# Optimization experiments

Measured on AMD Instinct MI355X. Metric: run time of the kernel, lower is better.

Reference implementation:

```python
import jax, jax.numpy as jnp
import numpy as np

EPS = 1e-16


def _euclidean_distance(x):
    # 'Euclidean Distance Matrix Trick' with the exact eps/mask handling of the torch code
    x2 = jnp.matmul(x, x.T)                      # [N, N]
    x2_norm = jnp.diag(x2)                       # [N]
    d = x2_norm[None, :] + x2_norm[:, None] - 2.0 * x2
    d = jax.nn.relu(d)
    mask = (d == 0.0).astype(d.dtype)
    d = d + mask * EPS
    d = jnp.sqrt(d + EPS) * (1.0 - mask) + EPS
    return d


def _valid_triplet_mask(labels):
    n = labels.shape[0]
    not_eye = ~jnp.eye(n, dtype=bool)            # [N, N]
    # distinct indices: i!=j, i!=k, j!=k
    distinct = not_eye[:, :, None] & not_eye[:, None, :] & not_eye[None, :, :]
    same = labels[None, :] == labels[:, None]    # [N, N]
    # label(i)==label(j) and label(i)!=label(k)
    valid = same[:, :, None] & ~same[:, None, :]
    return distinct & valid


def setup_inputs() -> dict:
    key = jax.random.key(0)
    k1, k2 = jax.random.split(key)
    N, D = 512, 128
    embeddings = jax.random.normal(k1, (N, D), dtype=jnp.float32)
    labels = jax.random.randint(k2, (N,), 0, 64, dtype=jnp.int64)
    bias = jnp.zeros((1,), dtype=jnp.float32)
    return {"embeddings": embeddings, "labels": labels, "bias": bias}


def reference(embeddings, labels, bias):
    distance = _euclidean_distance(embeddings)           # [N, N]
    # loss[i,j,k] = d(i,j) - d(i,k) + bias
    loss = distance[:, :, None] - distance[:, None, :] + bias[0]
    mask = _valid_triplet_mask(labels).astype(loss.dtype)
    loss = jax.nn.relu(loss * mask)
    num_positives = jnp.sum(loss > 1e-16).astype(loss.dtype)
    return jnp.sum(loss) / (num_positives + 1e-16)
```

## Files before the change

kernel.cpp:

```cpp
#include <hip/hip_runtime.h>

#define NPTS 512
#define DIM  128
#define EPSF 1e-16f
#define SROW 132

__global__ __launch_bounds__(512) void distmat(
    const float* __restrict__ X,
    float* __restrict__ D)
{
    __shared__ float A[32 * SROW];
    __shared__ float B[32 * SROW];
    __shared__ float nA[32], nB[32];

    const int bi = blockIdx.x & 15;
    const int bj = blockIdx.x >> 4;
    const int r0 = bi * 32, c0 = bj * 32;
    const int t = threadIdx.x;

    for (int g = t; g < 1024; g += 512) {
        const int r = g >> 5, c4 = g & 31;
        *reinterpret_cast<float4*>(&A[r * SROW + c4 * 4]) =
            reinterpret_cast<const float4*>(X + (size_t)(r0 + r) * DIM)[c4];
        *reinterpret_cast<float4*>(&B[r * SROW + c4 * 4]) =
            reinterpret_cast<const float4*>(X + (size_t)(c0 + r) * DIM)[c4];
    }
    __syncthreads();

    if (t < 64) {
        const float* src = (t < 32) ? &A[t * SROW] : &B[(t - 32) * SROW];
        float s = 0.f;
        for (int c4 = 0; c4 < 32; ++c4) {
            float4 v = *reinterpret_cast<const float4*>(src + c4 * 4);
            s += v.x * v.x + v.y * v.y + v.z * v.z + v.w * v.w;
        }
        if (t < 32) nA[t] = s; else nB[t - 32] = s;
    }
    __syncthreads();

    const int c  = t & 31;
    const int ty = t >> 5;
    float acc[2] = {0.f, 0.f};
    for (int k4 = 0; k4 < 32; ++k4) {
        const float4 bv = *reinterpret_cast<const float4*>(&B[c * SROW + k4 * 4]);
#pragma unroll
        for (int q = 0; q < 2; ++q) {
            const float4 av = *reinterpret_cast<const float4*>(&A[(ty + 16 * q) * SROW + k4 * 4]);
            acc[q] += av.x * bv.x + av.y * bv.y + av.z * bv.z + av.w * bv.w;
        }
    }
#pragma unroll
    for (int q = 0; q < 2; ++q) {
        const int r = ty + 16 * q;
        const float draw = fmaxf(nA[r] + nB[c] - 2.f * acc[q], 0.f);
        D[(size_t)(r0 + r) * NPTS + (c0 + c)] =
            (draw == 0.f) ? EPSF : (sqrtf(draw + EPSF) + EPSF);
    }
}

__global__ __launch_bounds__(512) void triplet_sum(
    const float* __restrict__ D,
    const int* __restrict__ labels,
    const float* __restrict__ bias,
    float* __restrict__ psum,
    unsigned* __restrict__ pcnt)
{
    __shared__ int      lab[NPTS];
    __shared__ float    drow[2][NPTS];
    __shared__ int      poslist[2][96];
    __shared__ int      npos[2];
    __shared__ float    wsum[8];
    __shared__ unsigned wcnt[8];

    const int blk = blockIdx.x;
    const int t   = threadIdx.x;
    const int i0  = blk * 2;

    lab[t] = labels[t];
    if (t < 256) {
        reinterpret_cast<float4*>(&drow[0][0])[t] =
            reinterpret_cast<const float4*>(D + (size_t)i0 * NPTS)[t];
    }
    if (t < 2) npos[t] = 0;
    __syncthreads();

    const int li0 = lab[i0], li1 = lab[i0 + 1];
    {
        const int j = t;
        if (lab[j] == li0 && j != i0)     { int q = atomicAdd(&npos[0], 1); poslist[0][q] = j; }
        if (lab[j] == li1 && j != i0 + 1) { int q = atomicAdd(&npos[1], 1); poslist[1][q] = j; }
    }
    __syncthreads();
    if (t < 2) {
        const int n = npos[t];
        for (int a2 = 1; a2 < n; ++a2) {
            int v = poslist[t][a2];
            int b2 = a2 - 1;
            while (b2 >= 0 && poslist[t][b2] > v) { poslist[t][b2 + 1] = poslist[t][b2]; --b2; }
            poslist[t][b2 + 1] = v;
        }
    }
    __syncthreads();

    const float bv = bias[0];
    float    lsum = 0.f;
    unsigned lcnt = 0u;
#pragma unroll
    for (int a = 0; a < 2; ++a) {
        const int   la = lab[i0 + a];
        const float* dr = &drow[a][0];
        if (lab[t] != la) {
            const float dik = dr[t];
            const int n = npos[a];
            for (int q = 0; q < n; ++q) {
                const float s = dr[poslist[a][q]] - dik + bv;
                if (s > 0.f) { lsum += s; lcnt += (s > EPSF) ? 1u : 0u; }
            }
        }
    }

#pragma unroll
    for (int off = 32; off > 0; off >>= 1) {
        lsum += __shfl_down(lsum, off);
        lcnt += __shfl_down(lcnt, off);
    }
    if ((t & 63) == 0) { wsum[t >> 6] = lsum; wcnt[t >> 6] = lcnt; }
    __syncthreads();
    if (t == 0) {
        float s = 0.f; unsigned c = 0u;
#pragma unroll
        for (int w = 0; w < 8; ++w) { s += wsum[w]; c += wcnt[w]; }
        psum[blk] = s;
        pcnt[blk] = c;
    }
}

__global__ __launch_bounds__(256) void triplet_finalize(
    const float* __restrict__ psum,
    const unsigned* __restrict__ pcnt,
    float* __restrict__ out)
{
    __shared__ float    ss[256];
    __shared__ unsigned sc[256];
    const int t = threadIdx.x;
    ss[t] = psum[t];
    sc[t] = pcnt[t];
    __syncthreads();
    for (int off = 128; off > 0; off >>= 1) {
        if (t < off) { ss[t] += ss[t + off]; sc[t] += sc[t + off]; }
        __syncthreads();
    }
    if (t == 0) out[0] = ss[0] / ((float)sc[0] + 1e-16f);
}

extern "C" void kernel_launch(void* const* d_in, const int* in_sizes, int n_in,
                              void* d_out, int out_size, void* d_ws, size_t ws_size,
                              hipStream_t stream) {
    const float* X      = (const float*)d_in[0];
    const int*   labels = (const int*)d_in[1];
    const float* bias   = (const float*)d_in[2];
    float*       out    = (float*)d_out;

    float*    D    = (float*)d_ws;
    float*    psum = (float*)((char*)d_ws + NPTS * NPTS * 4);
    unsigned* pcnt = (unsigned*)((char*)psum + 256 * 4);

    distmat<<<256, 512, 0, stream>>>(X, D);
    triplet_sum<<<256, 512, 0, stream>>>(D, labels, bias, psum, pcnt);
    triplet_finalize<<<1, 256, 0, stream>>>(psum, pcnt, out);
}
```

Before: 21.75 us.

## Fuse distance-matrix computation into triplet kernel and shuffle-reduce finalize

Removes the separate distmat kernel and global distance matrix; each triplet block now computes its two distance rows directly from X, using 4 threads per column j with shuffle reductions. This drops one launch and the write and re-read of a 1 MB matrix. In exchange each block re-reads all of X (256 KB, L2-resident) and recomputes the column norms, so total FLOPs are duplicated across blocks. The finalize kernel is also reduced to a single wavefront using shuffles instead of a shared-memory tree.

```diff
diff --git a/kernel.cpp b/kernel.cpp
--- a/kernel.cpp
+++ b/kernel.cpp
@@ -3,63 +3,9 @@
 #define NPTS 512
 #define DIM  128
 #define EPSF 1e-16f
-#define SROW 132
 
-__global__ __launch_bounds__(512) void distmat(
+__global__ __launch_bounds__(512) void triplet_fused(
     const float* __restrict__ X,
-    float* __restrict__ D)
-{
-    __shared__ float A[32 * SROW];
-    __shared__ float B[32 * SROW];
-    __shared__ float nA[32], nB[32];
-
-    const int bi = blockIdx.x & 15;
-    const int bj = blockIdx.x >> 4;
-    const int r0 = bi * 32, c0 = bj * 32;
-    const int t = threadIdx.x;
-
-    for (int g = t; g < 1024; g += 512) {
-        const int r = g >> 5, c4 = g & 31;
-        *reinterpret_cast<float4*>(&A[r * SROW + c4 * 4]) =
-            reinterpret_cast<const float4*>(X + (size_t)(r0 + r) * DIM)[c4];
-        *reinterpret_cast<float4*>(&B[r * SROW + c4 * 4]) =
-            reinterpret_cast<const float4*>(X + (size_t)(c0 + r) * DIM)[c4];
-    }
-    __syncthreads();
-
-    if (t < 64) {
-        const float* src = (t < 32) ? &A[t * SROW] : &B[(t - 32) * SROW];
-        float s = 0.f;
-        for (int c4 = 0; c4 < 32; ++c4) {
-            float4 v = *reinterpret_cast<const float4*>(src + c4 * 4);
-            s += v.x * v.x + v.y * v.y + v.z * v.z + v.w * v.w;
-        }
-        if (t < 32) nA[t] = s; else nB[t - 32] = s;
-    }
-    __syncthreads();
-
-    const int c  = t & 31;
-    const int ty = t >> 5;
-    float acc[2] = {0.f, 0.f};
-    for (int k4 = 0; k4 < 32; ++k4) {
-        const float4 bv = *reinterpret_cast<const float4*>(&B[c * SROW + k4 * 4]);
-#pragma unroll
-        for (int q = 0; q < 2; ++q) {
-            const float4 av = *reinterpret_cast<const float4*>(&A[(ty + 16 * q) * SROW + k4 * 4]);
-            acc[q] += av.x * bv.x + av.y * bv.y + av.z * bv.z + av.w * bv.w;
-        }
-    }
-#pragma unroll
-    for (int q = 0; q < 2; ++q) {
-        const int r = ty + 16 * q;
-        const float draw = fmaxf(nA[r] + nB[c] - 2.f * acc[q], 0.f);
-        D[(size_t)(r0 + r) * NPTS + (c0 + c)] =
-            (draw == 0.f) ? EPSF : (sqrtf(draw + EPSF) + EPSF);
-    }
-}
-
-__global__ __launch_bounds__(512) void triplet_sum(
-    const float* __restrict__ D,
     const int* __restrict__ labels,
     const float* __restrict__ bias,
     float* __restrict__ psum,
@@ -67,6 +13,7 @@
 {
     __shared__ int      lab[NPTS];
     __shared__ float    drow[2][NPTS];
+    __shared__ float4   xi4[2][DIM / 4];
     __shared__ int      poslist[2][96];
     __shared__ int      npos[2];
     __shared__ float    wsum[8];
@@ -77,11 +24,53 @@
     const int i0  = blk * 2;
 
     lab[t] = labels[t];
-    if (t < 256) {
-        reinterpret_cast<float4*>(&drow[0][0])[t] =
-            reinterpret_cast<const float4*>(D + (size_t)i0 * NPTS)[t];
+    if (t < 64) {
+        const int a = t >> 5, c4 = t & 31;
+        xi4[a][c4] = reinterpret_cast<const float4*>(X + (size_t)(i0 + a) * DIM)[c4];
     }
     if (t < 2) npos[t] = 0;
+    __syncthreads();
+
+    const int jl = t >> 2;
+    const int ch = t & 3;
+
+    float4 w0[8], w1[8];
+#pragma unroll
+    for (int m = 0; m < 8; ++m) { w0[m] = xi4[0][ch + 4 * m]; w1[m] = xi4[1][ch + 4 * m]; }
+
+    float n0 = 0.f, n1 = 0.f;
+#pragma unroll
+    for (int m = 0; m < 8; ++m) {
+        float4 a = w0[m], b = w1[m];
+        n0 += a.x * a.x + a.y * a.y + a.z * a.z + a.w * a.w;
+        n1 += b.x * b.x + b.y * b.y + b.z * b.z + b.w * b.w;
+    }
+    n0 += __shfl_xor(n0, 1); n0 += __shfl_xor(n0, 2);
+    n1 += __shfl_xor(n1, 1); n1 += __shfl_xor(n1, 2);
+
+#pragma unroll
+    for (int q = 0; q < 4; ++q) {
+        const int j = q * 128 + jl;
+        const float4* xj = reinterpret_cast<const float4*>(X + (size_t)j * DIM);
+        float d0 = 0.f, d1 = 0.f, nj = 0.f;
+#pragma unroll
+        for (int m = 0; m < 8; ++m) {
+            const float4 v = xj[ch + 4 * m];
+            const float4 a = w0[m], b = w1[m];
+            d0 += v.x * a.x + v.y * a.y + v.z * a.z + v.w * a.w;
+            d1 += v.x * b.x + v.y * b.y + v.z * b.z + v.w * b.w;
+            nj += v.x * v.x + v.y * v.y + v.z * v.z + v.w * v.w;
+        }
+        d0 += __shfl_xor(d0, 1); d0 += __shfl_xor(d0, 2);
+        d1 += __shfl_xor(d1, 1); d1 += __shfl_xor(d1, 2);
+        nj += __shfl_xor(nj, 1); nj += __shfl_xor(nj, 2);
+        if (ch == 0) {
+            const float r0 = fmaxf(n0 + nj - 2.f * d0, 0.f);
+            const float r1 = fmaxf(n1 + nj - 2.f * d1, 0.f);
+            drow[0][j] = (r0 == 0.f) ? EPSF : (sqrtf(r0 + EPSF) + EPSF);
+            drow[1][j] = (r1 == 0.f) ? EPSF : (sqrtf(r1 + EPSF) + EPSF);
+        }
+    }
     __syncthreads();
 
     const int li0 = lab[i0], li1 = lab[i0 + 1];
@@ -107,7 +96,7 @@
     unsigned lcnt = 0u;
 #pragma unroll
     for (int a = 0; a < 2; ++a) {
-        const int   la = lab[i0 + a];
+        const int    la = lab[i0 + a];
         const float* dr = &drow[a][0];
         if (lab[t] != la) {
             const float dik = dr[t];
@@ -135,22 +124,20 @@
     }
 }
 
-__global__ __launch_bounds__(256) void triplet_finalize(
+__global__ __launch_bounds__(64) void triplet_finalize(
     const float* __restrict__ psum,
     const unsigned* __restrict__ pcnt,
     float* __restrict__ out)
 {
-    __shared__ float    ss[256];
-    __shared__ unsigned sc[256];
     const int t = threadIdx.x;
-    ss[t] = psum[t];
-    sc[t] = pcnt[t];
-    __syncthreads();
-    for (int off = 128; off > 0; off >>= 1) {
-        if (t < off) { ss[t] += ss[t + off]; sc[t] += sc[t + off]; }
-        __syncthreads();
+    float    s = psum[t] + psum[t + 64] + psum[t + 128] + psum[t + 192];
+    unsigned c = pcnt[t] + pcnt[t + 64] + pcnt[t + 128] + pcnt[t + 192];
+#pragma unroll
+    for (int off = 32; off > 0; off >>= 1) {
+        s += __shfl_down(s, off);
+        c += __shfl_down(c, off);
     }
-    if (t == 0) out[0] = ss[0] / ((float)sc[0] + 1e-16f);
+    if (t == 0) out[0] = s / ((float)c + 1e-16f);
 }
 
 extern "C" void kernel_launch(void* const* d_in, const int* in_sizes, int n_in,
@@ -161,11 +148,9 @@
     const float* bias   = (const float*)d_in[2];
     float*       out    = (float*)d_out;
 
-    float*    D    = (float*)d_ws;
-    float*    psum = (float*)((char*)d_ws + NPTS * NPTS * 4);
-    unsigned* pcnt = (unsigned*)((char*)psum + 256 * 4);
+    float*    psum = (float*)d_ws;
+    unsigned* pcnt = (unsigned*)((char*)d_ws + 256 * 4);
 
-    distmat<<<256, 512, 0, stream>>>(X, D);
-    triplet_sum<<<256, 512, 0, stream>>>(D, labels, bias, psum, pcnt);
-    triplet_finalize<<<1, 256, 0, stream>>>(psum, pcnt, out);
+    triplet_fused<<<256, 512, 0, stream>>>(X, labels, bias, psum, pcnt);
+    triplet_finalize<<<1, 64, 0, stream>>>(psum, pcnt, out);
 }
```

New measurement: 20.28 us (median of 2 runs). -6.8%, faster.
